# Kernel tuning notes

Measured on AMD Instinct MI355X. Metric: run time of the kernel, lower is better.

The kernel has to match this reference:

```python
import jax, jax.numpy as jnp
import numpy as np

V, E, HD, T, B, S = 32000, 256, 512, 9, 64, 512
H = HD // 2
PAD = 0
NEG = -10000.0


def setup_inputs() -> dict:
    key = jax.random.key(0)
    ks = jax.random.split(key, 12)
    # right-padded variable-length sequences (pack_padded_sequence semantics)
    lengths = jax.random.randint(ks[0], (B,), S // 4, S + 1)
    attention_mask = jnp.arange(S)[None, :] < lengths[:, None]  # [B,S] bool
    input_ids = jax.random.randint(ks[1], (B, S), 1, V)
    input_ids = jnp.where(attention_mask, input_ids, 0)
    sc = 1.0 / np.sqrt(H)
    embed_table = jax.random.normal(ks[2], (V, E), jnp.float32) * 0.02
    embed_table = embed_table.at[PAD].set(0.0)  # padding_idx=0
    u = lambda k, shp: jax.random.uniform(k, shp, jnp.float32, -sc, sc)
    Wih_f, Whh_f, b_f = u(ks[3], (4 * H, E)), u(ks[4], (4 * H, H)), u(ks[5], (4 * H,))
    Wih_r, Whh_r, b_r = u(ks[6], (4 * H, E)), u(ks[7], (4 * H, H)), u(ks[8], (4 * H,))
    W_out, b_out = u(ks[9], (T, HD)), u(ks[10], (T,))
    transitions = jax.random.normal(ks[11], (T, T), jnp.float32)
    transitions = transitions.at[PAD, :].set(NEG).at[:, PAD].set(NEG)
    return dict(input_ids=input_ids, attention_mask=attention_mask,
                embed_table=embed_table, Wih_f=Wih_f, Whh_f=Whh_f, b_f=b_f,
                Wih_r=Wih_r, Whh_r=Whh_r, b_r=b_r, W_out=W_out, b_out=b_out,
                transitions=transitions)


def _lstm_dir(x, m, Wih, Whh, b, reverse):
    """x: [S,B,E] time-major, m: [S,B] bool. Returns h outputs [S,B,H].
    Masked steps freeze (h,c), matching packed-sequence behavior for
    right-padded inputs in both scan directions."""
    Hh = Whh.shape[1]
    def step(carry, inp):
        h, c = carry
        xt, mt = inp
        g = xt @ Wih.T + h @ Whh.T + b                    # [B,4H]
        i, f, gg, o = jnp.split(g, 4, axis=-1)            # torch gate order i,f,g,o
        cn = jax.nn.sigmoid(f) * c + jax.nn.sigmoid(i) * jnp.tanh(gg)
        hn = jax.nn.sigmoid(o) * jnp.tanh(cn)
        mt = mt[:, None]
        return (jnp.where(mt, hn, h), jnp.where(mt, cn, c)), jnp.where(mt, hn, h)
    h0 = jnp.zeros((x.shape[1], Hh), x.dtype)
    _, hs = jax.lax.scan(step, (h0, h0), (x, m), reverse=reverse)
    return hs


def reference(input_ids, attention_mask, embed_table, Wih_f, Whh_f, b_f,
              Wih_r, Whh_r, b_r, W_out, b_out, transitions):
    mask = attention_mask.astype(bool)
    x = embed_table[input_ids].transpose(1, 0, 2)         # [S,B,E] time-major
    m = mask.T                                            # [S,B]
    hf = _lstm_dir(x, m, Wih_f, Whh_f, b_f, reverse=False)
    hr = _lstm_dir(x, m, Wih_r, Whh_r, b_r, reverse=True)
    hs = jnp.concatenate([hf, hr], axis=-1) * m[:, :, None]  # zero pads (pad_packed)
    feats = hs @ W_out.T + b_out                          # [S,B,T]
    # Viterbi forward pass
    v0 = jnp.full((feats.shape[1], T), NEG, feats.dtype).at[:, PAD].set(0.0)
    def vstep(v, inp):
        f_t, m_t = inp
        scores = v[:, :, None] + transitions[None]        # [B, from, to]
        bp = jnp.argmax(scores, axis=1)                   # [B,T]
        best = jnp.take_along_axis(scores, bp[:, None, :], axis=1)[:, 0, :] + f_t
        return jnp.where(m_t[:, None], best, v), bp
    v, bps = jax.lax.scan(vstep, v0, (feats, m))          # bps [S,B,T]
    last = jnp.argmax(v + transitions[PAD], axis=1)       # [B]
    # backtrace: path[i] = where(mask[i+1], bp[i+1][path[i+1]], 0)
    def bstep(tag, inp):
        bp_t, m_t = inp
        prev = jnp.take_along_axis(bp_t, tag[:, None], axis=1)[:, 0]
        prev = jnp.where(m_t, prev, 0)
        return prev, prev
    _, path_rest = jax.lax.scan(bstep, last, (bps[1:], m[1:]), reverse=True)
    return jnp.concatenate([path_rest, last[None]], axis=0).T  # [B,S]
```

## Files before the change

### kernel.cpp

```cpp
#include <hip/hip_runtime.h>


#define SLEN 512
#define NTAG 9
#define NEGV -10000.0f

typedef float f32x2 __attribute__((ext_vector_type(2)));
typedef float f32x4 __attribute__((ext_vector_type(4)));

__device__ __forceinline__ float qsum(float v){
  int t = __builtin_amdgcn_update_dpp(0, __float_as_int(v), 0xB1, 0xF, 0xF, false);
  v += __int_as_float(t);
  t = __builtin_amdgcn_update_dpp(0, __float_as_int(v), 0x4E, 0xF, 0xF, false);
  return v + __int_as_float(t);
}
__device__ __forceinline__ float rsum16(float v){
  v = qsum(v);
  int t = __builtin_amdgcn_update_dpp(0, __float_as_int(v), 0x124, 0xF, 0xF, false);
  v += __int_as_float(t);
  t = __builtin_amdgcn_update_dpp(0, __float_as_int(v), 0x128, 0xF, 0xF, false);
  return v + __int_as_float(t);
}

#define MAC2(S, WP, HV) { \
  f32x2 _h01{(HV).x,(HV).y}, _h23{(HV).z,(HV).w}; \
  asm("v_pk_fma_f32 %0, %1, %2, %0 op_sel:[0,0,0] op_sel_hi:[0,1,1]" : "+v"(S) : "v"(WP), "v"(_h01)); \
  asm("v_pk_fma_f32 %0, %1, %2, %0 op_sel:[1,0,0] op_sel_hi:[1,1,1]" : "+v"(S) : "v"(WP), "v"(_h23)); }

#define LDW(rr,kq,A,B) { f32x4 v = wp[((rr)*4+(kq))*1024 + t]; A = f32x2{v.x,v.y}; B = f32x2{v.z,v.w}; }

#define DECLW \
  f32x2 w00,w01,w02,w03,w04,w05,w06,w07; \
  f32x2 w10,w11,w12,w13,w14,w15,w16,w17; \
  f32x2 w20,w21,w22,w23,w24,w25,w26,w27; \
  f32x2 w30,w31,w32,w33,w34,w35,w36,w37; \
  LDW(0,0,w00,w01) LDW(0,1,w02,w03) LDW(0,2,w04,w05) LDW(0,3,w06,w07) \
  LDW(1,0,w10,w11) LDW(1,1,w12,w13) LDW(1,2,w14,w15) LDW(1,3,w16,w17) \
  LDW(2,0,w20,w21) LDW(2,1,w22,w23) LDW(2,2,w24,w25) LDW(2,3,w26,w27) \
  LDW(3,0,w30,w31) LDW(3,1,w32,w33) LDW(3,2,w34,w35) LDW(3,3,w36,w37)

#define PINW \
  asm volatile("" : "+v"(w00),"+v"(w01),"+v"(w02),"+v"(w03),"+v"(w04),"+v"(w05),"+v"(w06),"+v"(w07)); \
  asm volatile("" : "+v"(w10),"+v"(w11),"+v"(w12),"+v"(w13),"+v"(w14),"+v"(w15),"+v"(w16),"+v"(w17)); \
  asm volatile("" : "+v"(w20),"+v"(w21),"+v"(w22),"+v"(w23),"+v"(w24),"+v"(w25),"+v"(w26),"+v"(w27)); \
  asm volatile("" : "+v"(w30),"+v"(w31),"+v"(w32),"+v"(w33),"+v"(w34),"+v"(w35),"+v"(w36),"+v"(w37));

#define GCHUNK(c, WA0,WA1, WB0,WB1, WC0,WC1, WD0,WD1) { \
  f32x4 hA = *(const f32x4*)(hb + (c)*8); \
  f32x4 hB = *(const f32x4*)(hb + (c)*8 + 4); \
  MAC2(s0,WA0,hA) MAC2(s0,WA1,hB) \
  MAC2(s1,WB0,hA) MAC2(s1,WB1,hB) \
  MAC2(s2,WC0,hA) MAC2(s2,WC1,hB) \
  MAC2(s3,WD0,hA) MAC2(s3,WD1,hB) }

#define GEMV4x16 \
  f32x2 s0{0.f,0.f}, s1{0.f,0.f}, s2{0.f,0.f}, s3{0.f,0.f}; \
  GCHUNK(0, w00,w01, w10,w11, w20,w21, w30,w31) \
  GCHUNK(1, w02,w03, w12,w13, w22,w23, w32,w33) \
  GCHUNK(2, w04,w05, w14,w15, w24,w25, w34,w35) \
  GCHUNK(3, w06,w07, w16,w17, w26,w27, w36,w37)

union PK { struct { float v; int tg; } s; unsigned long long u; };

__global__ void prep_k(const float* __restrict__ wihf, const float* __restrict__ whhf,
                       const float* __restrict__ wihr, const float* __restrict__ whhr,
                       float* __restrict__ wS){
  for (int i = blockIdx.x*blockDim.x + threadIdx.x; i < (1<<20); i += gridDim.x*blockDim.x){
    int e=i&3, t=(i>>2)&1023, inst=(i>>12)&15, g=(i>>16)&3, d=(i>>18)&1, role=(i>>19)&1;
    int rr = inst>>2, kq = inst&3;
    int row = g*256 + (t>>4)*4 + rr;
    int k   = (t&15)*16 + kq*4 + e;
    const float* s = role ? (d? whhr : whhf) : (d? wihr : wihf);
    wS[i] = s[row*256 + k];
  }
}

__global__ __launch_bounds__(1024)
__attribute__((amdgpu_waves_per_eu(4,4)))
void xproj_k(
    int c0, int Sc,
    const int* __restrict__ ids, const float* __restrict__ embed,
    const float* __restrict__ wS,
    const float* __restrict__ bias_f, const float* __restrict__ bias_r,
    float* __restrict__ xg, long xg_par_str)
{
  __shared__ __align__(16) float xl2[2][576];
  __shared__ int ids_l[1024];
  const int t = threadIdx.x;
  const int bid = blockIdx.x;
  const int bp = bid & 31, g = (bid>>5)&3, d = bid>>7;
  const int rg = t>>4, ks = t&15;

  const f32x4* wp = (const f32x4*)(wS + (long)((d*4+g)*16)*4096);
  DECLW
  PINW
  const float bbr = (d ? bias_r : bias_f)[g*256 + rg*4 + (ks&3)];

  for (int i=t; i<2*Sc; i+=1024){
    int b = (i>=Sc) ? 1 : 0, sp = i - b*Sc;
    int sg = d ? (SLEN-1-(c0*Sc+sp)) : (c0*Sc+sp);
    ids_l[i] = ids[(bp*2+b)*SLEN + sg];
  }
  __syncthreads();
  const int bl = t&1, kk = t>>1;
  if (t < 128){
    f32x4 v = ((const f32x4*)embed)[(long)ids_l[bl*Sc]*64 + kk];
    #pragma unroll
    for (int ii=0; ii<4; ii++){
      int k = kk*4+ii;
      xl2[0][(k>>4)*36 + (k&15)*2 + bl] = v[ii];
    }
  }
  __syncthreads();
  float* xgb = xg + (long)(c0&1)*xg_par_str;
  const float* hb = xl2[0] + ks*36;
  for (int sp=0; sp<Sc; sp++){
    f32x4 pfv;
    const bool hpf = (sp+1 < Sc) && (t < 128);
    if (hpf) pfv = ((const f32x4*)embed)[(long)ids_l[bl*Sc + sp+1]*64 + kk];
    hb = xl2[sp&1] + ks*36;
    GEMV4x16
    float r0a = rsum16(s0.x), r0b = rsum16(s0.y);
    float r1a = rsum16(s1.x), r1b = rsum16(s1.y);
    float r2a = rsum16(s2.x), r2b = rsum16(s2.y);
    float r3a = rsum16(s3.x), r3b = rsum16(s3.y);
    if (ks < 4){
      float ra = (ks==0)?r0a:(ks==1)?r1a:(ks==2)?r2a:r3a;
      float rb = (ks==0)?r0b:(ks==1)?r1b:(ks==2)?r2b:r3b;
      int j = rg*4 + ks;
      long base = ((long)(d*Sc+sp)*64 + bp*2)*1024 + g*256 + j;
      xgb[base]        = ra + bbr;
      xgb[base + 1024] = rb + bbr;
    }
    if (hpf){
      #pragma unroll
      for (int ii=0; ii<4; ii++){
        int k = kk*4+ii;
        xl2[(sp+1)&1][(k>>4)*36 + (k&15)*2 + bl] = pfv[ii];
      }
    }
    __syncthreads();
  }
}

__global__ __launch_bounds__(1024)
__attribute__((amdgpu_waves_per_eu(4,4)))
void recur_k(
    int c0, int Sc,
    const int* __restrict__ ids,
    const float* __restrict__ wS,
    const float* __restrict__ xg, long xg_par_str,
    float* __restrict__ hs,
    float* __restrict__ st_h, float* __restrict__ st_c,
    unsigned long long* __restrict__ send)
{
  __shared__ __align__(16) float hl2[576];
  __shared__ float ol[2][256];
  __shared__ int ml[1024];
  const int t = threadIdx.x;
  const int bid = blockIdx.x;
  const int g = (bid>>3)&3;
  const int grp = (bid&7) | ((bid>>5)<<3);
  const int d = grp>>5, bp = grp&31;
  const int rg = t>>4, ks = t&15;

  const f32x4* wp = (const f32x4*)(wS + (long)(((2+d)*4+g)*16)*4096);
  DECLW
  PINW

  for (int i=t; i<2*Sc; i+=1024){
    int b = (i>=Sc) ? 1 : 0, sp = i - b*Sc;
    int sg = d ? (SLEN-1-(c0*Sc+sp)) : (c0*Sc+sp);
    ml[i] = ids[(bp*2+b)*SLEN + sg];
  }
  float cst = 0.f, hpv = 0.f;
  const int j2 = t&255, b2 = t>>8;
  if (t < 512){
    int bg = bp*2 + b2;
    hpv = st_h[(d*64+bg)*256 + j2];
    cst = st_c[(d*64+bg)*256 + j2];
    hl2[(j2>>4)*36 + (j2&15)*2 + b2] = hpv;
  }
  __syncthreads();
  const float* xgb = xg + (long)(c0&1)*xg_par_str;
  const float* hb = hl2 + ks*36;
  const int g1 = (g+1)&3, g2c = (g+2)&3, g3 = (g+3)&3;

  for (int sp=0; sp<Sc; sp++){
    const int stepg = c0*Sc + sp;
    const int par = stepg & 1;
    const int target = stepg + 1;
    float x0=0,x1=0,x2=0,x3=0;
    if (t < 512){
      const float* xr = xgb + ((long)(d*Sc+sp)*64 + (bp*2+b2))*1024 + j2;
      x0 = xr[0]; x1 = xr[256]; x2 = xr[512]; x3 = xr[768];
    }
    GEMV4x16
    float r0a = rsum16(s0.x), r0b = rsum16(s0.y);
    float r1a = rsum16(s1.x), r1b = rsum16(s1.y);
    float r2a = rsum16(s2.x), r2b = rsum16(s2.y);
    float r3a = rsum16(s3.x), r3b = rsum16(s3.y);
    if (ks < 4){
      float ra = (ks==0)?r0a:(ks==1)?r1a:(ks==2)?r2a:r3a;
      float rb = (ks==0)?r0b:(ks==1)?r1b:(ks==2)?r2b:r3b;
      int j = rg*4 + ks;
      ol[0][j] = ra; ol[1][j] = rb;
      PK pa; pa.s.v = ra; pa.s.tg = target;
      PK pb; pb.s.v = rb; pb.s.tg = target;
      unsigned long long* sb = send + ((((long)(par*64+grp)*4 + g)*2)*256) + j;
      __hip_atomic_store(sb,       pa.u, __ATOMIC_RELAXED, __HIP_MEMORY_SCOPE_AGENT);
      __hip_atomic_store(sb + 256, pb.u, __ATOMIC_RELAXED, __HIP_MEMORY_SCOPE_AGENT);
    }
    __syncthreads();
    if (t < 512){
      const unsigned long long* rbase =
          send + (long)(par*64+grp)*4*2*256 + b2*256 + j2;
      PK u1, u2, u3;
      u1.u = __hip_atomic_load(rbase + (long)g1*512,  __ATOMIC_RELAXED, __HIP_MEMORY_SCOPE_AGENT);
      u2.u = __hip_atomic_load(rbase + (long)g2c*512, __ATOMIC_RELAXED, __HIP_MEMORY_SCOPE_AGENT);
      u3.u = __hip_atomic_load(rbase + (long)g3*512,  __ATOMIC_RELAXED, __HIP_MEMORY_SCOPE_AGENT);
      int cnt = 0;
      while (u1.s.tg < target || u2.s.tg < target || u3.s.tg < target){
        if (u1.s.tg < target) u1.u = __hip_atomic_load(rbase + (long)g1*512,  __ATOMIC_RELAXED, __HIP_MEMORY_SCOPE_AGENT);
        if (u2.s.tg < target) u2.u = __hip_atomic_load(rbase + (long)g2c*512, __ATOMIC_RELAXED, __HIP_MEMORY_SCOPE_AGENT);
        if (u3.s.tg < target) u3.u = __hip_atomic_load(rbase + (long)g3*512,  __ATOMIC_RELAXED, __HIP_MEMORY_SCOPE_AGENT);
        if (++cnt > (1<<15)) break;
      }
      float vo = ol[b2][j2];
      float a0,a1,a2,a3;
      if      (g==0){ a0=vo;     a1=u1.s.v; a2=u2.s.v; a3=u3.s.v; }
      else if (g==1){ a1=vo;     a2=u1.s.v; a3=u2.s.v; a0=u3.s.v; }
      else if (g==2){ a2=vo;     a3=u1.s.v; a0=u2.s.v; a1=u3.s.v; }
      else          { a3=vo;     a0=u1.s.v; a1=u2.s.v; a2=u3.s.v; }
      float pi = a0 + x0, pf = a1 + x1, pg = a2 + x2, po = a3 + x3;
      float ii = 1.f/(1.f+expf(-pi)), ff = 1.f/(1.f+expf(-pf));
      float gv = tanhf(pg),           oo = 1.f/(1.f+expf(-po));
      float cn = ff*cst + ii*gv;
      float hn = oo*tanhf(cn);
      if (ml[b2*Sc+sp] != 0){ cst = cn; hpv = hn; }
      hl2[(j2>>4)*36 + (j2&15)*2 + b2] = hpv;
      if (g == 0){
        int sg = d ? (SLEN-1-stepg) : stepg;
        hs[((long)sg*64 + (bp*2+b2))*512 + d*256 + j2] = hpv;
      }
    }
    __syncthreads();
  }
  if (t < 512){
    int bg = bp*2 + b2;
    st_h[(d*64+bg)*256 + j2] = hpv;
    st_c[(d*64+bg)*256 + j2] = cst;
  }
}

__global__ __launch_bounds__(576) void feats_k(
    const float* __restrict__ hs, const float* __restrict__ wout,
    float* __restrict__ feats)
{
  __shared__ __align__(16) float hlds[64*512];
  __shared__ __align__(16) float wl[NTAG*512];
  const int s = blockIdx.x, t = threadIdx.x;
  for (int i = t; i < 64*512/4; i += 576)
    ((f32x4*)hlds)[i] = ((const f32x4*)(hs + (long)s*64*512))[i];
  for (int i = t; i < NTAG*512/4; i += 576)
    ((f32x4*)wl)[i] = ((const f32x4*)wout)[i];
  __syncthreads();
  int b = t / 9, tag = t - b*9;
  float acc = 0.f;
  const float* hb = hlds + b*512;
  const float* wb = wl + tag*512;
  for (int k=0; k<512; k+=4){
    f32x4 h4 = *(const f32x4*)(hb+k);
    f32x4 w4 = *(const f32x4*)(wb+k);
    acc += h4.x*w4.x + h4.y*w4.y + h4.z*w4.z + h4.w*w4.w;
  }
  feats[((long)s*64 + b)*9 + tag] = acc;
}

__global__ __launch_bounds__(64) void viterbi_k(
    const int* __restrict__ ids, const float* __restrict__ feats,
    const float* __restrict__ bout, const float* __restrict__ trans,
    int* __restrict__ outp)
{
  __shared__ float fl[SLEN*NTAG + 64];
  __shared__ unsigned char bps[SLEN*NTAG];
  __shared__ unsigned char mk[SLEN];
  const int b = blockIdx.x, lane = threadIdx.x;
  for (int i=lane; i<SLEN; i+=64) mk[i] = (ids[b*SLEN+i] != 0) ? 1 : 0;
  for (int i=lane; i<SLEN*NTAG; i+=64){
    int s = i/9; int t = i - s*9;
    fl[i] = feats[((long)s*64+b)*9 + t] + bout[t];
  }
  fl[SLEN*NTAG + lane] = 0.f;
  __syncthreads();

  float Tc[9], v[9], vown;
  #pragma unroll
  for (int i=0;i<9;i++) Tc[i] = (lane<9)? trans[i*9 + lane] : 0.f;
  #pragma unroll
  for (int i=0;i<9;i++) v[i] = (i==0)?0.f:NEGV;
  vown = (lane==0)?0.f:NEGV;

  for (int s=0;s<SLEN;s++){
    float best = v[0] + Tc[0]; int bi = 0;
    #pragma unroll
    for (int i=1;i<9;i++){
      float sc = v[i] + Tc[i];
      if (sc > best){ best = sc; bi = i; }
    }
    float nv = best + fl[s*9 + lane];
    bool m = mk[s] != 0;
    if (m && lane<9) vown = nv;
    if (lane < 9) bps[s*9+lane] = (unsigned char)bi;
    #pragma unroll
    for (int i=0;i<9;i++) v[i] = __shfl(vown, i);
  }
  if (lane == 0){
    float best = v[0]; int tag = 0;
    #pragma unroll
    for (int i=1;i<9;i++) if (v[i] > best){ best=v[i]; tag=i; }
    outp[b*SLEN + SLEN-1] = tag;
    for (int t=SLEN-1; t>=1; t--){
      int pv = bps[t*9 + tag];
      if (!mk[t]) pv = 0;
      outp[b*SLEN + t-1] = pv;
      tag = pv;
    }
  }
}

extern "C" void kernel_launch(void* const* d_in, const int* in_sizes, int n_in,
                              void* d_out, int out_size, void* d_ws, size_t ws_size,
                              hipStream_t stream){
  (void)in_sizes; (void)n_in; (void)out_size;
  const int*   ids   = (const int*)  d_in[0];
  const float* embed = (const float*)d_in[2];
  const float* Wih_f = (const float*)d_in[3];
  const float* Whh_f = (const float*)d_in[4];
  const float* b_f   = (const float*)d_in[5];
  const float* Wih_r = (const float*)d_in[6];
  const float* Whh_r = (const float*)d_in[7];
  const float* b_r   = (const float*)d_in[8];
  const float* Wout  = (const float*)d_in[9];
  const float* bout  = (const float*)d_in[10];
  const float* trans = (const float*)d_in[11];

  float* fw = (float*)d_ws;
  size_t off = 0;
  float* wS    = fw + off; off += 1048576;
  unsigned long long* send = (unsigned long long*)(fw + off); off += 524288;
  float* st_h  = fw + off; off += 32768;
  float* st_c  = fw + off; off += 32768;
  float* hs    = fw + off; off += 16777216;
  float* featb = fw + off; off += 294912;
  float* xg    = fw + off;
  size_t fixedB = off*4;

  const int cands[7] = {512,256,128,64,32,16,8};
  int Sc = 8;
  for (int ci=0; ci<7; ci++){
    size_t need = fixedB + (size_t)cands[ci]*262144*4;
    if (need <= ws_size){ Sc = cands[ci]; break; }
  }
  const long xg_par_str = (long)Sc*131072;
  const int C = SLEN / Sc;

  hipMemsetAsync(send, 0, 524288*4, stream);
  hipMemsetAsync(st_h, 0, 2*32768*4, stream);
  prep_k<<<1024,256,0,stream>>>(Wih_f, Whh_f, Wih_r, Whh_r, wS);
  for (int c0=0; c0<C; c0++){
    xproj_k<<<256,1024,0,stream>>>(c0, Sc, ids, embed, wS, b_f, b_r, xg, xg_par_str);
    recur_k<<<256,1024,0,stream>>>(c0, Sc, ids, wS, xg, xg_par_str, hs, st_h, st_c, send);
  }
  feats_k<<<512,576,0,stream>>>(hs, Wout, featb);
  viterbi_k<<<64,64,0,stream>>>(ids, featb, bout, trans, (int*)d_out);
}
```

Before: 1.989 ms.

## Batch embedding staging in xproj and drop a barrier per recurrent step

The input-projection kernel now stages up to 64 timesteps of embeddings into a large shared buffer at once, which removes the per-step barrier and prefetch. It also spreads the output writes over 8 lanes per row group instead of 4. In the recurrent kernel, each lane that does the cell update takes its own reduced gate value straight from registers instead of going through shared memory. The hidden-state buffer is double-buffered, so one __syncthreads per step goes away. The costs are a much larger shared-memory footprint in xproj, which may limit occupancy, and the cell update now being spread across threads in a different pattern.

```diff
diff --git a/kernel.cpp b/kernel.cpp
--- a/kernel.cpp
+++ b/kernel.cpp
@@ -84,62 +84,51 @@
     const float* __restrict__ bias_f, const float* __restrict__ bias_r,
     float* __restrict__ xg, long xg_par_str)
 {
-  __shared__ __align__(16) float xl2[2][576];
+  __shared__ __align__(16) float xbig[64][576];
   __shared__ int ids_l[1024];
   const int t = threadIdx.x;
   const int bid = blockIdx.x;
   const int bp = bid & 31, g = (bid>>5)&3, d = bid>>7;
   const int rg = t>>4, ks = t&15;
+  const int e = ks&3, bu = (ks>>2)&1;
 
   const f32x4* wp = (const f32x4*)(wS + (long)((d*4+g)*16)*4096);
   DECLW
   PINW
-  const float bbr = (d ? bias_r : bias_f)[g*256 + rg*4 + (ks&3)];
+  const float bbr = (d ? bias_r : bias_f)[g*256 + rg*4 + e];
 
   for (int i=t; i<2*Sc; i+=1024){
     int b = (i>=Sc) ? 1 : 0, sp = i - b*Sc;
     int sg = d ? (SLEN-1-(c0*Sc+sp)) : (c0*Sc+sp);
     ids_l[i] = ids[(bp*2+b)*SLEN + sg];
   }
-  __syncthreads();
-  const int bl = t&1, kk = t>>1;
-  if (t < 128){
-    f32x4 v = ((const f32x4*)embed)[(long)ids_l[bl*Sc]*64 + kk];
-    #pragma unroll
-    for (int ii=0; ii<4; ii++){
-      int k = kk*4+ii;
-      xl2[0][(k>>4)*36 + (k&15)*2 + bl] = v[ii];
-    }
-  }
-  __syncthreads();
+  const int SH = (Sc < 64) ? Sc : 64;
   float* xgb = xg + (long)(c0&1)*xg_par_str;
-  const float* hb = xl2[0] + ks*36;
-  for (int sp=0; sp<Sc; sp++){
-    f32x4 pfv;
-    const bool hpf = (sp+1 < Sc) && (t < 128);
-    if (hpf) pfv = ((const f32x4*)embed)[(long)ids_l[bl*Sc + sp+1]*64 + kk];
-    hb = xl2[sp&1] + ks*36;
-    GEMV4x16
-    float r0a = rsum16(s0.x), r0b = rsum16(s0.y);
-    float r1a = rsum16(s1.x), r1b = rsum16(s1.y);
-    float r2a = rsum16(s2.x), r2b = rsum16(s2.y);
-    float r3a = rsum16(s3.x), r3b = rsum16(s3.y);
-    if (ks < 4){
-      float ra = (ks==0)?r0a:(ks==1)?r1a:(ks==2)?r2a:r3a;
-      float rb = (ks==0)?r0b:(ks==1)?r1b:(ks==2)?r2b:r3b;
-      int j = rg*4 + ks;
-      long base = ((long)(d*Sc+sp)*64 + bp*2)*1024 + g*256 + j;
-      xgb[base]        = ra + bbr;
-      xgb[base + 1024] = rb + bbr;
-    }
-    if (hpf){
-      #pragma unroll
-      for (int ii=0; ii<4; ii++){
-        int k = kk*4+ii;
-        xl2[(sp+1)&1][(k>>4)*36 + (k&15)*2 + bl] = pfv[ii];
+
+  for (int sp0=0; sp0<Sc; sp0+=SH){
+    __syncthreads();
+    for (int c = t; c < SH*128; c += 1024){
+      int ss = c>>7, b = (c>>6)&1, kk = c&63;
+      int sp = sp0 + ss;
+      f32x4 v = ((const f32x4*)embed)[(long)ids_l[b*Sc+sp]*64 + kk];
+      float* xb = &xbig[ss][(kk>>2)*36 + (kk&3)*8 + b];
+      xb[0] = v.x; xb[2] = v.y; xb[4] = v.z; xb[6] = v.w;
+    }
+    __syncthreads();
+    for (int sp=sp0; sp<sp0+SH; sp++){
+      const float* hb = &xbig[sp-sp0][ks*36];
+      GEMV4x16
+      float r0a = rsum16(s0.x), r0b = rsum16(s0.y);
+      float r1a = rsum16(s1.x), r1b = rsum16(s1.y);
+      float r2a = rsum16(s2.x), r2b = rsum16(s2.y);
+      float r3a = rsum16(s3.x), r3b = rsum16(s3.y);
+      if (ks < 8){
+        float va = (e==0)?r0a:(e==1)?r1a:(e==2)?r2a:r3a;
+        float vb = (e==0)?r0b:(e==1)?r1b:(e==2)?r2b:r3b;
+        long base = ((long)(d*Sc+sp)*64 + (bp*2+bu))*1024 + g*256 + rg*4 + e;
+        xgb[base] = (bu ? vb : va) + bbr;
       }
     }
-    __syncthreads();
   }
 }
 
@@ -154,8 +143,7 @@
     float* __restrict__ st_h, float* __restrict__ st_c,
     unsigned long long* __restrict__ send)
 {
-  __shared__ __align__(16) float hl2[576];
-  __shared__ float ol[2][256];
+  __shared__ __align__(16) float hl2[2][576];
   __shared__ int ml[1024];
   const int t = threadIdx.x;
   const int bid = blockIdx.x;
@@ -163,6 +151,10 @@
   const int grp = (bid&7) | ((bid>>5)<<3);
   const int d = grp>>5, bp = grp&31;
   const int rg = t>>4, ks = t&15;
+  const int e = ks&3, bu = (ks>>2)&1;
+  const bool upd = (ks < 8);
+  const int ju = rg*4 + e;
+  const int bg = bp*2 + bu;
 
   const f32x4* wp = (const f32x4*)(wS + (long)(((2+d)*4+g)*16)*4096);
   DECLW
@@ -174,16 +166,13 @@
     ml[i] = ids[(bp*2+b)*SLEN + sg];
   }
   float cst = 0.f, hpv = 0.f;
-  const int j2 = t&255, b2 = t>>8;
-  if (t < 512){
-    int bg = bp*2 + b2;
-    hpv = st_h[(d*64+bg)*256 + j2];
-    cst = st_c[(d*64+bg)*256 + j2];
-    hl2[(j2>>4)*36 + (j2&15)*2 + b2] = hpv;
+  if (upd){
+    hpv = st_h[(d*64+bg)*256 + ju];
+    cst = st_c[(d*64+bg)*256 + ju];
+    hl2[0][(ju>>4)*36 + (ju&15)*2 + bu] = hpv;
   }
   __syncthreads();
   const float* xgb = xg + (long)(c0&1)*xg_par_str;
-  const float* hb = hl2 + ks*36;
   const int g1 = (g+1)&3, g2c = (g+2)&3, g3 = (g+3)&3;
 
   for (int sp=0; sp<Sc; sp++){
@@ -191,10 +180,11 @@
     const int par = stepg & 1;
     const int target = stepg + 1;
     float x0=0,x1=0,x2=0,x3=0;
-    if (t < 512){
-      const float* xr = xgb + ((long)(d*Sc+sp)*64 + (bp*2+b2))*1024 + j2;
+    if (upd){
+      const float* xr = xgb + ((long)(d*Sc+sp)*64 + bg)*1024 + ju;
       x0 = xr[0]; x1 = xr[256]; x2 = xr[512]; x3 = xr[768];
     }
+    const float* hb = &hl2[sp&1][ks*36];
     GEMV4x16
     float r0a = rsum16(s0.x), r0b = rsum16(s0.y);
     float r1a = rsum16(s1.x), r1b = rsum16(s1.y);
@@ -204,17 +194,18 @@
       float ra = (ks==0)?r0a:(ks==1)?r1a:(ks==2)?r2a:r3a;
       float rb = (ks==0)?r0b:(ks==1)?r1b:(ks==2)?r2b:r3b;
       int j = rg*4 + ks;
-      ol[0][j] = ra; ol[1][j] = rb;
       PK pa; pa.s.v = ra; pa.s.tg = target;
       PK pb; pb.s.v = rb; pb.s.tg = target;
       unsigned long long* sb = send + ((((long)(par*64+grp)*4 + g)*2)*256) + j;
       __hip_atomic_store(sb,       pa.u, __ATOMIC_RELAXED, __HIP_MEMORY_SCOPE_AGENT);
       __hip_atomic_store(sb + 256, pb.u, __ATOMIC_RELAXED, __HIP_MEMORY_SCOPE_AGENT);
     }
-    __syncthreads();
-    if (t < 512){
+    if (upd){
+      float voa = (e==0)?r0a:(e==1)?r1a:(e==2)?r2a:r3a;
+      float vob = (e==0)?r0b:(e==1)?r1b:(e==2)?r2b:r3b;
+      float vo  = bu ? vob : voa;
       const unsigned long long* rbase =
-          send + (long)(par*64+grp)*4*2*256 + b2*256 + j2;
+          send + (long)(par*64+grp)*4*2*256 + bu*256 + ju;
       PK u1, u2, u3;
       u1.u = __hip_atomic_load(rbase + (long)g1*512,  __ATOMIC_RELAXED, __HIP_MEMORY_SCOPE_AGENT);
       u2.u = __hip_atomic_load(rbase + (long)g2c*512, __ATOMIC_RELAXED, __HIP_MEMORY_SCOPE_AGENT);
@@ -226,7 +217,6 @@
         if (u3.s.tg < target) u3.u = __hip_atomic_load(rbase + (long)g3*512,  __ATOMIC_RELAXED, __HIP_MEMORY_SCOPE_AGENT);
         if (++cnt > (1<<15)) break;
       }
-      float vo = ol[b2][j2];
       float a0,a1,a2,a3;
       if      (g==0){ a0=vo;     a1=u1.s.v; a2=u2.s.v; a3=u3.s.v; }
       else if (g==1){ a1=vo;     a2=u1.s.v; a3=u2.s.v; a0=u3.s.v; }
@@ -237,19 +227,18 @@
       float gv = tanhf(pg),           oo = 1.f/(1.f+expf(-po));
       float cn = ff*cst + ii*gv;
       float hn = oo*tanhf(cn);
-      if (ml[b2*Sc+sp] != 0){ cst = cn; hpv = hn; }
-      hl2[(j2>>4)*36 + (j2&15)*2 + b2] = hpv;
+      if (ml[bu*Sc+sp] != 0){ cst = cn; hpv = hn; }
+      hl2[(sp+1)&1][(ju>>4)*36 + (ju&15)*2 + bu] = hpv;
       if (g == 0){
         int sg = d ? (SLEN-1-stepg) : stepg;
-        hs[((long)sg*64 + (bp*2+b2))*512 + d*256 + j2] = hpv;
+        hs[((long)sg*64 + bg)*512 + d*256 + ju] = hpv;
       }
     }
     __syncthreads();
   }
-  if (t < 512){
-    int bg = bp*2 + b2;
-    st_h[(d*64+bg)*256 + j2] = hpv;
-    st_c[(d*64+bg)*256 + j2] = cst;
+  if (upd){
+    st_h[(d*64+bg)*256 + ju] = hpv;
+    st_c[(d*64+bg)*256 + ju] = cst;
   }
 }
 
```

After: 2.273 ms. 1.14x slower.

## Batch embedding staging in xproj and use fast exp/rcp activations in recurrence

Applied to the files above, without the earlier changes.

The input projection kernel now stages up to 64 timesteps of embeddings into a large shared buffer per batch, then runs the GEMVs back to back with no per-step barrier. Stores are spread across 8 lanes instead of 4. The recurrent kernel replaces expf/tanhf with hardware v_exp_f32/v_rcp_f32 approximations for sigmoid and tanh, which shortens the serial per-step critical path. In exchange, shared memory use grows to about 147KB, which may limit occupancy, and the activations lose some accuracy.

```diff
diff --git a/kernel.cpp b/kernel.cpp
--- a/kernel.cpp
+++ b/kernel.cpp
@@ -20,6 +20,19 @@
   v += __int_as_float(t);
   t = __builtin_amdgcn_update_dpp(0, __float_as_int(v), 0x128, 0xF, 0xF, false);
   return v + __int_as_float(t);
+}
+
+__device__ __forceinline__ float fexp2(float x){
+  float r; asm("v_exp_f32 %0, %1" : "=v"(r) : "v"(x)); return r;
+}
+__device__ __forceinline__ float frcp(float x){
+  float r; asm("v_rcp_f32 %0, %1" : "=v"(r) : "v"(x)); return r;
+}
+__device__ __forceinline__ float fsigm(float x){
+  return frcp(1.0f + fexp2(-1.4426950408889634f * x));
+}
+__device__ __forceinline__ float ftanh(float x){
+  return fmaf(2.0f, frcp(1.0f + fexp2(-2.8853900817779268f * x)), -1.0f);
 }
 
 #define MAC2(S, WP, HV) { \
@@ -84,62 +97,51 @@
     const float* __restrict__ bias_f, const float* __restrict__ bias_r,
     float* __restrict__ xg, long xg_par_str)
 {
-  __shared__ __align__(16) float xl2[2][576];
+  __shared__ __align__(16) float xbig[64][576];
   __shared__ int ids_l[1024];
   const int t = threadIdx.x;
   const int bid = blockIdx.x;
   const int bp = bid & 31, g = (bid>>5)&3, d = bid>>7;
   const int rg = t>>4, ks = t&15;
+  const int e = ks&3, bu = (ks>>2)&1;
 
   const f32x4* wp = (const f32x4*)(wS + (long)((d*4+g)*16)*4096);
   DECLW
   PINW
-  const float bbr = (d ? bias_r : bias_f)[g*256 + rg*4 + (ks&3)];
+  const float bbr = (d ? bias_r : bias_f)[g*256 + rg*4 + e];
 
   for (int i=t; i<2*Sc; i+=1024){
     int b = (i>=Sc) ? 1 : 0, sp = i - b*Sc;
     int sg = d ? (SLEN-1-(c0*Sc+sp)) : (c0*Sc+sp);
     ids_l[i] = ids[(bp*2+b)*SLEN + sg];
   }
-  __syncthreads();
-  const int bl = t&1, kk = t>>1;
-  if (t < 128){
-    f32x4 v = ((const f32x4*)embed)[(long)ids_l[bl*Sc]*64 + kk];
-    #pragma unroll
-    for (int ii=0; ii<4; ii++){
-      int k = kk*4+ii;
-      xl2[0][(k>>4)*36 + (k&15)*2 + bl] = v[ii];
-    }
-  }
-  __syncthreads();
+  const int SH = (Sc < 64) ? Sc : 64;
   float* xgb = xg + (long)(c0&1)*xg_par_str;
-  const float* hb = xl2[0] + ks*36;
-  for (int sp=0; sp<Sc; sp++){
-    f32x4 pfv;
-    const bool hpf = (sp+1 < Sc) && (t < 128);
-    if (hpf) pfv = ((const f32x4*)embed)[(long)ids_l[bl*Sc + sp+1]*64 + kk];
-    hb = xl2[sp&1] + ks*36;
-    GEMV4x16
-    float r0a = rsum16(s0.x), r0b = rsum16(s0.y);
-    float r1a = rsum16(s1.x), r1b = rsum16(s1.y);
-    float r2a = rsum16(s2.x), r2b = rsum16(s2.y);
-    float r3a = rsum16(s3.x), r3b = rsum16(s3.y);
-    if (ks < 4){
-      float ra = (ks==0)?r0a:(ks==1)?r1a:(ks==2)?r2a:r3a;
-      float rb = (ks==0)?r0b:(ks==1)?r1b:(ks==2)?r2b:r3b;
-      int j = rg*4 + ks;
-      long base = ((long)(d*Sc+sp)*64 + bp*2)*1024 + g*256 + j;
-      xgb[base]        = ra + bbr;
-      xgb[base + 1024] = rb + bbr;
-    }
-    if (hpf){
-      #pragma unroll
-      for (int ii=0; ii<4; ii++){
-        int k = kk*4+ii;
-        xl2[(sp+1)&1][(k>>4)*36 + (k&15)*2 + bl] = pfv[ii];
+
+  for (int sp0=0; sp0<Sc; sp0+=SH){
+    __syncthreads();
+    for (int c = t; c < SH*128; c += 1024){
+      int ss = c>>7, b = (c>>6)&1, kk = c&63;
+      int sp = sp0 + ss;
+      f32x4 v = ((const f32x4*)embed)[(long)ids_l[b*Sc+sp]*64 + kk];
+      float* xb = &xbig[ss][(kk>>2)*36 + (kk&3)*8 + b];
+      xb[0] = v.x; xb[2] = v.y; xb[4] = v.z; xb[6] = v.w;
+    }
+    __syncthreads();
+    for (int sp=sp0; sp<sp0+SH; sp++){
+      const float* hb = &xbig[sp-sp0][ks*36];
+      GEMV4x16
+      float r0a = rsum16(s0.x), r0b = rsum16(s0.y);
+      float r1a = rsum16(s1.x), r1b = rsum16(s1.y);
+      float r2a = rsum16(s2.x), r2b = rsum16(s2.y);
+      float r3a = rsum16(s3.x), r3b = rsum16(s3.y);
+      if (ks < 8){
+        float va = (e==0)?r0a:(e==1)?r1a:(e==2)?r2a:r3a;
+        float vb = (e==0)?r0b:(e==1)?r1b:(e==2)?r2b:r3b;
+        long base = ((long)(d*Sc+sp)*64 + (bp*2+bu))*1024 + g*256 + rg*4 + e;
+        xgb[base] = (bu ? vb : va) + bbr;
       }
     }
-    __syncthreads();
   }
 }
 
@@ -233,10 +235,10 @@
       else if (g==2){ a2=vo;     a3=u1.s.v; a0=u2.s.v; a1=u3.s.v; }
       else          { a3=vo;     a0=u1.s.v; a1=u2.s.v; a2=u3.s.v; }
       float pi = a0 + x0, pf = a1 + x1, pg = a2 + x2, po = a3 + x3;
-      float ii = 1.f/(1.f+expf(-pi)), ff = 1.f/(1.f+expf(-pf));
-      float gv = tanhf(pg),           oo = 1.f/(1.f+expf(-po));
+      float ii = fsigm(pi), ff = fsigm(pf);
+      float gv = ftanh(pg), oo = fsigm(po);
       float cn = ff*cst + ii*gv;
-      float hn = oo*tanhf(cn);
+      float hn = oo*ftanh(cn);
       if (ml[b2*Sc+sp] != 0){ cst = cn; hpv = hn; }
       hl2[(j2>>4)*36 + (j2&15)*2 + b2] = hpv;
       if (g == 0){
```

After: 1.841 ms. 1.08x faster.
